# Kernel optimization log

Hardware: AMD Instinct MI355X
Metric: run time of the kernel (lower is better)

## Reference

```python
import jax, jax.numpy as jnp
import numpy as np

N = 100000
E = 1600000
G = 64  # number of graphs
H = 128
BN_EPS = 1e-5


def setup_inputs() -> dict:
    key = jax.random.key(0)
    ks = jax.random.split(key, 12)
    x = jax.random.normal(ks[0], (N, 3), dtype=jnp.float32)
    edge_index = jax.random.randint(ks[1], (2, E), 0, N, dtype=jnp.int64)
    batch = jnp.sort(jax.random.randint(ks[2], (N,), 0, G, dtype=jnp.int64))
    W1 = jax.random.normal(ks[3], (3, H), dtype=jnp.float32) * 0.3
    W2 = jax.random.normal(ks[4], (H, H), dtype=jnp.float32) * 0.05
    W3 = jax.random.normal(ks[5], (H, H), dtype=jnp.float32) * 0.05
    lin_W = jax.random.normal(ks[6], (H, 2), dtype=jnp.float32) * 0.05
    d = {
        'x': x, 'edge_index': edge_index, 'batch': batch,
        'W1': W1, 'b1': jnp.zeros((H,), jnp.float32),
        'W2': W2, 'b2': jnp.zeros((H,), jnp.float32),
        'W3': W3, 'b3': jnp.zeros((H,), jnp.float32),
        'lin_W': lin_W, 'lin_b': jnp.zeros((2,), jnp.float32),
    }
    for i, kk in zip((1, 2, 3), ks[7:10]):
        d[f'bn{i}_g'] = jnp.ones((H,), jnp.float32)
        d[f'bn{i}_b'] = jnp.zeros((H,), jnp.float32)
        d[f'bn{i}_m'] = jnp.zeros((H,), jnp.float32)
        d[f'bn{i}_v'] = jax.random.uniform(kk, (H,), dtype=jnp.float32, minval=0.5, maxval=1.5)
    return d


def _gcn(x, src, dst, norm, W, b):
    # GCNConv: out = scatter_add(norm * (xW)[src], dst) + b
    h = x @ W
    msg = h[src] * norm[:, None]
    agg = jax.ops.segment_sum(msg, dst, num_segments=N)
    return agg + b


def _bn_eval(x, g, b, m, v):
    return (x - m) * jax.lax.rsqrt(v + BN_EPS) * g + b


def reference(x, edge_index, batch, W1, b1, W2, b2, W3, b3,
              bn1_g, bn1_b, bn1_m, bn1_v,
              bn2_g, bn2_b, bn2_m, bn2_v,
              bn3_g, bn3_b, bn3_m, bn3_v,
              lin_W, lin_b):
    loop = jnp.arange(N, dtype=edge_index.dtype)
    src = jnp.concatenate([edge_index[0], loop])
    dst = jnp.concatenate([edge_index[1], loop])
    # symmetric normalization with self-loops: deg from destination nodes
    deg = jax.ops.segment_sum(jnp.ones_like(dst, dtype=x.dtype), dst, num_segments=N)
    dinv = jnp.where(deg > 0, jax.lax.rsqrt(deg), 0.0)
    norm = dinv[src] * dinv[dst]

    h = jax.nn.relu(_bn_eval(_gcn(x, src, dst, norm, W1, b1), bn1_g, bn1_b, bn1_m, bn1_v))
    h = jax.nn.relu(_bn_eval(_gcn(h, src, dst, norm, W2, b2), bn2_g, bn2_b, bn2_m, bn2_v))
    h = jax.nn.relu(_bn_eval(_gcn(h, src, dst, norm, W3, b3), bn3_g, bn3_b, bn3_m, bn3_v))
    # dropout is identity in eval mode
    sums = jax.ops.segment_sum(h, batch, num_segments=G)
    cnts = jax.ops.segment_sum(jnp.ones((N,), h.dtype), batch, num_segments=G)
    pooled = sums / jnp.maximum(cnts, 1.0)[:, None]
    return pooled @ lin_W + lin_b
```

## Files before the change

### kernel.cpp

```cpp
#include <hip/hip_runtime.h>

#define NN 100000
#define EE 1600000
#define GG 64
#define HH 128
#define BN_EPS 1e-5f

#define CB 782
#define NB 256
#define TILE 6250

typedef unsigned short ushort_t;

static __device__ inline ushort_t f2bf(float f) {
    unsigned u = __float_as_uint(f);
    unsigned r = (u + 0x7FFF + ((u >> 16) & 1)) >> 16;
    return (ushort_t)r;
}
static __device__ inline float bf2f(ushort_t b) {
    return __uint_as_float(((unsigned)b) << 16);
}


__global__ __launch_bounds__(256) void k_hist(const int* __restrict__ ei,
                                              int* __restrict__ histG) {
    __shared__ int h[CB];
    int t = threadIdx.x;
    for (int i = t; i < CB; i += 256) h[i] = 0;
    __syncthreads();
    int e0 = blockIdx.x * TILE;
    for (int i = t; i < TILE; i += 256) {
        int d = ei[EE + e0 + i];
        atomicAdd(&h[d >> 7], 1);
    }
    __syncthreads();
    for (int i = t; i < CB; i += 256) histG[blockIdx.x * CB + i] = h[i];
}

__global__ __launch_bounds__(NB) void k_bscan(int* __restrict__ histG,
                                              int* __restrict__ total) {
    __shared__ int sh[NB];
    int t = threadIdx.x;
    int c = blockIdx.x;
    sh[t] = histG[t * CB + c];
    __syncthreads();
    for (int d = 1; d < NB; d <<= 1) {
        int x = (t >= d) ? sh[t - d] : 0;
        __syncthreads();
        sh[t] += x;
        __syncthreads();
    }
    histG[t * CB + c] = (t > 0) ? sh[t - 1] : 0;
    if (t == NB - 1) total[c] = sh[NB - 1];
}

__global__ __launch_bounds__(1024) void k_cbase(const int* __restrict__ total,
                                                int* __restrict__ cbase) {
    __shared__ int sh[1024];
    int t = threadIdx.x;
    sh[t] = (t < CB) ? total[t] : 0;
    __syncthreads();
    for (int d = 1; d < 1024; d <<= 1) {
        int x = (t >= d) ? sh[t - d] : 0;
        __syncthreads();
        sh[t] += x;
        __syncthreads();
    }
    if (t < CB) cbase[t] = (t > 0) ? sh[t - 1] : 0;
    if (t == CB - 1) cbase[CB] = sh[t];
}

__global__ __launch_bounds__(256) void k_cscatter(const int* __restrict__ ei,
                                                  const int* __restrict__ histG,
                                                  const int* __restrict__ cbase,
                                                  int* __restrict__ metaS) {
    __shared__ int base_l[CB];
    __shared__ int cur_l[CB];
    int t = threadIdx.x;
    int b = blockIdx.x;
    for (int i = t; i < CB; i += 256) {
        base_l[i] = cbase[i] + histG[b * CB + i];
        cur_l[i] = 0;
    }
    __syncthreads();
    int e0 = b * TILE;
    for (int i = t; i < TILE; i += 256) {
        int s = ei[e0 + i];
        int d = ei[EE + e0 + i];
        int c = d >> 7;
        int p = base_l[c] + atomicAdd(&cur_l[c], 1);
        metaS[p] = s | ((d & 127) << 17);
    }
}

__global__ __launch_bounds__(256) void k_fine(const int* __restrict__ metaS,
                                              const int* __restrict__ cbase,
                                              int* __restrict__ cnt,
                                              int* __restrict__ offs,
                                              int* __restrict__ col,
                                              float* __restrict__ dinv) {
    __shared__ int hist[128];
    __shared__ int scn[128];
    __shared__ int cur[128];
    int t = threadIdx.x;
    int c = blockIdx.x;
    int lo = cbase[c], hi = cbase[c + 1];
    if (t < 128) hist[t] = 0;
    __syncthreads();
    for (int r = lo + t; r < hi; r += 256) atomicAdd(&hist[metaS[r] >> 17], 1);
    __syncthreads();
    if (t < 128) scn[t] = hist[t];
    __syncthreads();
    for (int d = 1; d < 128; d <<= 1) {
        int x = (t >= d && t < 128) ? scn[t - d] : 0;
        __syncthreads();
        if (t < 128) scn[t] += x;
        __syncthreads();
    }
    if (t < 128) {
        int excl = (t > 0) ? scn[t - 1] : 0;
        cur[t] = excl;
        int node = c * 128 + t;
        if (node < NN) {
            cnt[node] = hist[t];
            offs[node] = lo + excl;
            dinv[node] = rsqrtf((float)(hist[t] + 1));
        }
    }
    __syncthreads();
    for (int r = lo + t; r < hi; r += 256) {
        int pk = metaS[r];
        int s = pk & 0x1FFFF;
        int idx = atomicAdd(&cur[pk >> 17], 1);
        col[lo + idx] = s;
    }
}


__global__ __launch_bounds__(256) void k_aggx(const float* __restrict__ x,
                                              const int* __restrict__ offs,
                                              const int* __restrict__ cnt,
                                              const int* __restrict__ col,
                                              const float* __restrict__ dinv,
                                              float* __restrict__ wgt,
                                              float4* __restrict__ agg) {
    int tid = threadIdx.x;
    int wave = tid >> 6;
    int lane = tid & 63;
    int grp = lane >> 4;
    int l = lane & 15;
    int n = blockIdx.x * 16 + wave * 4 + grp;
    float dv = dinv[n];
    int base = offs[n], cn = cnt[n];
    float a0 = 0.f, a1 = 0.f, a2 = 0.f;
    for (int i = l; i < cn; i += 16) {
        int s = col[base + i];
        float w = dinv[s] * dv;
        wgt[base + i] = w;
        a0 += w * x[s * 3 + 0];
        a1 += w * x[s * 3 + 1];
        a2 += w * x[s * 3 + 2];
    }
#pragma unroll
    for (int off = 8; off >= 1; off >>= 1) {
        a0 += __shfl_xor(a0, off, 16);
        a1 += __shfl_xor(a1, off, 16);
        a2 += __shfl_xor(a2, off, 16);
    }
    if (l == 0) {
        float w0 = dv * dv;
        a0 += w0 * x[n * 3 + 0];
        a1 += w0 * x[n * 3 + 1];
        a2 += w0 * x[n * 3 + 2];
        agg[n] = make_float4(a0, a1, a2, 0.f);
    }
}


__global__ __launch_bounds__(256) void k_mml1(const float4* __restrict__ agg,
                                              const float* __restrict__ W1,
                                              const float* __restrict__ b1,
                                              const float* __restrict__ g1,
                                              const float* __restrict__ bb1,
                                              const float* __restrict__ m1,
                                              const float* __restrict__ v1,
                                              const float* __restrict__ W2,
                                              ushort_t* __restrict__ outB) {
    __shared__ float xs[64][132];
    __shared__ float4 ag[64];
    int tid = threadIdx.x;
    int row0 = blockIdx.x * 64;
    if (tid < 64) {
        int gr = row0 + tid;
        ag[tid] = (gr < NN) ? agg[gr] : make_float4(0.f, 0.f, 0.f, 0.f);
    }
    __syncthreads();
    {
        int c = tid & 127;
        int rh = tid >> 7;
        float w0 = W1[c], w1 = W1[128 + c], w2 = W1[256 + c];
        float sc = g1[c] * rsqrtf(v1[c] + BN_EPS);
        float sh = (b1[c] - m1[c]) * sc + bb1[c];
#pragma unroll
        for (int i = 0; i < 32; i++) {
            int r = 2 * i + rh;
            float4 a = ag[r];
            float t = a.x * w0 + a.y * w1 + a.z * w2;
            xs[r][c] = fmaxf(t * sc + sh, 0.f);
        }
    }
    __syncthreads();

    int tx = tid & 31;
    int ty = tid >> 5;
    float acc[8][4];
#pragma unroll
    for (int i = 0; i < 8; i++)
#pragma unroll
        for (int j = 0; j < 4; j++) acc[i][j] = 0.f;

    const float* Wp = W2 + tx * 4;
#pragma unroll 4
    for (int k = 0; k < 128; k++) {
        float4 w = *(const float4*)&Wp[k * HH];
#pragma unroll
        for (int i = 0; i < 8; i++) {
            float xv = xs[ty * 8 + i][k];
            acc[i][0] += xv * w.x;
            acc[i][1] += xv * w.y;
            acc[i][2] += xv * w.z;
            acc[i][3] += xv * w.w;
        }
    }
#pragma unroll
    for (int i = 0; i < 8; i++) {
        int gr = row0 + ty * 8 + i;
        if (gr < NN) {
            ushort4 o;
            o.x = f2bf(acc[i][0]);
            o.y = f2bf(acc[i][1]);
            o.z = f2bf(acc[i][2]);
            o.w = f2bf(acc[i][3]);
            *(ushort4*)&outB[(size_t)gr * HH + tx * 4] = o;
        }
    }
}


__global__ __launch_bounds__(256) void k_mm(const ushort_t* __restrict__ xin,
                                            const float* __restrict__ W,
                                            ushort_t* __restrict__ outB) {
    __shared__ float xs[64][132];
    int tid = threadIdx.x;
    int tx = tid & 31;
    int ty = tid >> 5;
    int row0 = blockIdx.x * 64;
#pragma unroll
    for (int i = 0; i < 4; i++) {
        int idx8 = i * 256 + tid;
        int r = idx8 >> 4;
        int k8 = (idx8 & 15) * 8;
        int gr = row0 + r;
        int4 pk = (gr < NN) ? *(const int4*)&xin[(size_t)gr * HH + k8]
                            : make_int4(0, 0, 0, 0);
        float* dst = &xs[r][k8];
        dst[0] = __uint_as_float(((unsigned)pk.x) << 16);
        dst[1] = __uint_as_float(((unsigned)pk.x) & 0xFFFF0000u);
        dst[2] = __uint_as_float(((unsigned)pk.y) << 16);
        dst[3] = __uint_as_float(((unsigned)pk.y) & 0xFFFF0000u);
        dst[4] = __uint_as_float(((unsigned)pk.z) << 16);
        dst[5] = __uint_as_float(((unsigned)pk.z) & 0xFFFF0000u);
        dst[6] = __uint_as_float(((unsigned)pk.w) << 16);
        dst[7] = __uint_as_float(((unsigned)pk.w) & 0xFFFF0000u);
    }
    __syncthreads();
    float acc[8][4];
#pragma unroll
    for (int i = 0; i < 8; i++)
#pragma unroll
        for (int j = 0; j < 4; j++) acc[i][j] = 0.f;

    const float* Wp = W + tx * 4;
#pragma unroll 4
    for (int k = 0; k < 128; k++) {
        float4 w = *(const float4*)&Wp[k * HH];
#pragma unroll
        for (int i = 0; i < 8; i++) {
            float xv = xs[ty * 8 + i][k];
            acc[i][0] += xv * w.x;
            acc[i][1] += xv * w.y;
            acc[i][2] += xv * w.z;
            acc[i][3] += xv * w.w;
        }
    }
#pragma unroll
    for (int i = 0; i < 8; i++) {
        int gr = row0 + ty * 8 + i;
        if (gr < NN) {
            ushort4 o;
            o.x = f2bf(acc[i][0]);
            o.y = f2bf(acc[i][1]);
            o.z = f2bf(acc[i][2]);
            o.w = f2bf(acc[i][3]);
            *(ushort4*)&outB[(size_t)gr * HH + tx * 4] = o;
        }
    }
}


__global__ __launch_bounds__(256) void k_agg(const ushort_t* __restrict__ t,
                                             const int* __restrict__ offs,
                                             const int* __restrict__ cnt,
                                             const int* __restrict__ col,
                                             const float* __restrict__ wgt,
                                             const float* __restrict__ dinv,
                                             const float* __restrict__ bias,
                                             const float* __restrict__ g,
                                             const float* __restrict__ bb,
                                             const float* __restrict__ m,
                                             const float* __restrict__ v,
                                             ushort_t* __restrict__ out) {
    int wave = threadIdx.x >> 6;
    int lane = threadIdx.x & 63;
    int half = lane >> 5;
    int l = lane & 31;
    int d = blockIdx.x * 8 + wave * 2 + half;
    int c0 = l * 4;
    float dv = dinv[d];
    float w0 = dv * dv;
    ushort4 selfR = *(const ushort4*)&t[(size_t)d * HH + c0];
    float4 acc;
    acc.x = bf2f(selfR.x) * w0; acc.y = bf2f(selfR.y) * w0;
    acc.z = bf2f(selfR.z) * w0; acc.w = bf2f(selfR.w) * w0;
    int base = offs[d], cn = cnt[d];
    for (int ib = 0; ib < cn; ib += 32) {
        int i = ib + l;
        int s = 0;
        float w = 0.f;
        if (i < cn) {
            s = col[base + i];
            w = wgt[base + i];
        }
        int lim = min(32, cn - ib);
#pragma unroll 8
        for (int j = 0; j < lim; j++) {
            int ss = __shfl(s, j, 32);
            float ww = __shfl(w, j, 32);
            ushort4 tv = *(const ushort4*)&t[(size_t)ss * HH + c0];
            acc.x += ww * bf2f(tv.x);
            acc.y += ww * bf2f(tv.y);
            acc.z += ww * bf2f(tv.z);
            acc.w += ww * bf2f(tv.w);
        }
    }
    float4 gg = *(const float4*)&g[c0];
    float4 vv = *(const float4*)&v[c0];
    float4 mm = *(const float4*)&m[c0];
    float4 bv = *(const float4*)&bb[c0];
    float4 bi = *(const float4*)&bias[c0];
    float sc0 = gg.x * rsqrtf(vv.x + BN_EPS);
    float sc1 = gg.y * rsqrtf(vv.y + BN_EPS);
    float sc2 = gg.z * rsqrtf(vv.z + BN_EPS);
    float sc3 = gg.w * rsqrtf(vv.w + BN_EPS);
    ushort4 o;
    o.x = f2bf(fmaxf(acc.x * sc0 + (bi.x - mm.x) * sc0 + bv.x, 0.f));
    o.y = f2bf(fmaxf(acc.y * sc1 + (bi.y - mm.y) * sc1 + bv.y, 0.f));
    o.z = f2bf(fmaxf(acc.z * sc2 + (bi.z - mm.z) * sc2 + bv.z, 0.f));
    o.w = f2bf(fmaxf(acc.w * sc3 + (bi.w - mm.w) * sc3 + bv.w, 0.f));
    *(ushort4*)&out[(size_t)d * HH + c0] = o;
}


#define PBLK 2048
__global__ void k_pool(const ushort_t* __restrict__ h, const int* __restrict__ batch,
                       float* __restrict__ gsum, int* __restrict__ gcnt) {
    int c = threadIdx.x;
    int per = (NN + PBLK - 1) / PBLK;
    int n0 = blockIdx.x * per;
    int n1 = min(NN, n0 + per);
    if (n0 >= NN) return;
    float acc = 0.f;
    int cur = batch[n0];
    int count = 0;
    for (int n = n0; n < n1; n++) {
        int gr = batch[n];
        if (gr != cur) {
            atomicAdd(&gsum[cur * HH + c], acc);
            if (c == 0) atomicAdd(&gcnt[cur], count);
            acc = 0.f; count = 0; cur = gr;
        }
        acc += bf2f(h[(size_t)n * HH + c]);
        count++;
    }
    atomicAdd(&gsum[cur * HH + c], acc);
    if (c == 0) atomicAdd(&gcnt[cur], count);
}

__global__ void k_head(const float* __restrict__ gsum, const int* __restrict__ gcnt,
                       const float* __restrict__ linW, const float* __restrict__ linb,
                       float* __restrict__ out) {
    int t = threadIdx.x;
    int gr = t >> 1, j = t & 1;
    float inv = 1.0f / fmaxf((float)gcnt[gr], 1.0f);
    float acc = 0.f;
    for (int c = 0; c < HH; c++) acc += gsum[gr * HH + c] * linW[c * 2 + j];
    out[t] = acc * inv + linb[j];
}


static inline size_t al256(size_t x) { return (x + 255) & ~(size_t)255; }

extern "C" void kernel_launch(void* const* d_in, const int* in_sizes, int n_in,
                              void* d_out, int out_size, void* d_ws, size_t ws_size,
                              hipStream_t stream) {
    const float* x    = (const float*)d_in[0];
    const int*   ei   = (const int*)d_in[1];
    const int*   batch= (const int*)d_in[2];
    const float* W1   = (const float*)d_in[3];
    const float* b1   = (const float*)d_in[4];
    const float* W2   = (const float*)d_in[5];
    const float* b2   = (const float*)d_in[6];
    const float* W3   = (const float*)d_in[7];
    const float* b3   = (const float*)d_in[8];
    const float* linW = (const float*)d_in[9];
    const float* linb = (const float*)d_in[10];
    const float* bn1g = (const float*)d_in[11];
    const float* bn1b = (const float*)d_in[12];
    const float* bn1m = (const float*)d_in[13];
    const float* bn1v = (const float*)d_in[14];
    const float* bn2g = (const float*)d_in[15];
    const float* bn2b = (const float*)d_in[16];
    const float* bn2m = (const float*)d_in[17];
    const float* bn2v = (const float*)d_in[18];
    const float* bn3g = (const float*)d_in[19];
    const float* bn3b = (const float*)d_in[20];
    const float* bn3m = (const float*)d_in[21];
    const float* bn3v = (const float*)d_in[22];
    float* out = (float*)d_out;

    char* ws = (char*)d_ws;
    size_t off = 0;
    int*    histG  = (int*)(ws + off);    off += al256((size_t)NB * CB * 4);
    int*    total  = (int*)(ws + off);    off += al256((size_t)CB * 4);
    int*    cbase  = (int*)(ws + off);    off += al256((size_t)(CB + 1) * 4);
    int*    cnt    = (int*)(ws + off);    off += al256((size_t)NN * 4);
    int*    offs   = (int*)(ws + off);    off += al256((size_t)NN * 4);
    float*  dinv   = (float*)(ws + off);  off += al256((size_t)NN * 4);
    int*    col    = (int*)(ws + off);    off += al256((size_t)EE * 4);
    float*  wgt    = (float*)(ws + off);  off += al256((size_t)EE * 4);
    float4* agg    = (float4*)(ws + off); off += al256((size_t)NN * 16);
    char*   bufA   = (char*)(ws + off);   off += al256((size_t)NN * HH * 2);
    char*   bufB   = (char*)(ws + off);   off += al256((size_t)NN * HH * 4);
    float*  gsum   = (float*)(ws + off);  off += (size_t)GG * HH * 4;
    int*    gcnt   = (int*)(ws + off);    off += al256((size_t)GG * 4);

    int* metaS = (int*)bufB;
    ushort_t* tB = (ushort_t*)bufB;
    ushort_t* hB = (ushort_t*)bufA;

    hipMemsetAsync(gsum, 0, (size_t)GG * HH * 4 + (size_t)GG * 4, stream);

    k_hist<<<NB, 256, 0, stream>>>(ei, histG);
    k_bscan<<<CB, NB, 0, stream>>>(histG, total);
    k_cbase<<<1, 1024, 0, stream>>>(total, cbase);
    k_cscatter<<<NB, 256, 0, stream>>>(ei, histG, cbase, metaS);
    k_fine<<<CB, 256, 0, stream>>>(metaS, cbase, cnt, offs, col, dinv);

    k_aggx<<<NN / 16, 256, 0, stream>>>(x, offs, cnt, col, dinv, wgt, agg);

    k_mml1<<<(NN + 63) / 64, 256, 0, stream>>>(agg, W1, b1, bn1g, bn1b, bn1m, bn1v,
                                               W2, tB);
    k_agg<<<NN / 8, 256, 0, stream>>>(tB, offs, cnt, col, wgt, dinv,
                                      b2, bn2g, bn2b, bn2m, bn2v, hB);

    k_mm<<<(NN + 63) / 64, 256, 0, stream>>>(hB, W3, tB);
    k_agg<<<NN / 8, 256, 0, stream>>>(tB, offs, cnt, col, wgt, dinv,
                                      b3, bn3g, bn3b, bn3m, bn3v, hB);

    k_pool<<<PBLK, 128, 0, stream>>>(hB, batch, gsum, gcnt);
    k_head<<<1, 128, 0, stream>>>(gsum, gcnt, linW, linb, out);
}
```

Measured before the change: 441.4 us.

## Use bf16 MFMA for dense layers, fuse pooling into last aggregation

Replaces the FP32 scalar GEMMs in the layer-1 and layer-3 matmul kernels with bf16 MFMA 16x16x32, using a split hi/lo bf16 representation to keep near-FP32 accuracy. Weights are pre-split into fragment layout by a new prep kernel. The aggregation kernel is restructured so each wave walks a contiguous range of nodes, with 16 lanes covering 128 channels and 4 neighbor groups. It computes edge weights on the fly instead of storing and reloading a wgt array, and the final layer's mean pooling is fused into it, removing the pool kernel. The extra MFMA passes for precision splitting and per-element scalar output stores add cost in exchange.

```diff
diff --git a/kernel.cpp b/kernel.cpp
--- a/kernel.cpp
+++ b/kernel.cpp
@@ -11,6 +11,12 @@
 #define TILE 6250
 
 typedef unsigned short ushort_t;
+typedef __attribute__((ext_vector_type(8))) short bf16x8;
+typedef __attribute__((ext_vector_type(4))) float f32x4;
+
+#define MFMA16 __builtin_amdgcn_mfma_f32_16x16x32_bf16
+
+#define WFRAG_LO 16384
 
 static __device__ inline ushort_t f2bf(float f) {
     unsigned u = __float_as_uint(f);
@@ -20,6 +26,8 @@
 static __device__ inline float bf2f(ushort_t b) {
     return __uint_as_float(((unsigned)b) << 16);
 }
+#define BFLO(u) __uint_as_float(((unsigned)(u)) << 16)
+#define BFHI(u) __uint_as_float(((unsigned)(u)) & 0xFFFF0000u)
 
 
 __global__ __launch_bounds__(256) void k_hist(const int* __restrict__ ei,
@@ -137,12 +145,43 @@
 }
 
 
+__global__ __launch_bounds__(256) void k_gcnt(const int* __restrict__ batch,
+                                              int* __restrict__ gcnt) {
+    int i = blockIdx.x * 256 + threadIdx.x;
+    if (i < NN) atomicAdd(&gcnt[batch[i]], 1);
+}
+
+
+__global__ __launch_bounds__(256) void k_wprep(const float* __restrict__ W2,
+                                               const float* __restrict__ W3,
+                                               ushort_t* __restrict__ w2f,
+                                               ushort_t* __restrict__ w3f) {
+    const float* W = (blockIdx.x & 8) ? W3 : W2;
+    ushort_t* o = (blockIdx.x & 8) ? w3f : w2f;
+    int tid = ((int)blockIdx.x & 7) * 256 + threadIdx.x;
+    int l = tid & 63;
+    int kb = ((tid >> 6) & 3) * 32 + (l >> 4) * 8;
+    int n = (tid >> 8) * 16 + (l & 15);
+    unsigned hp[4], lp[4];
+#pragma unroll
+    for (int p = 0; p < 4; p++) {
+        float v0 = W[(size_t)(kb + 2 * p) * HH + n];
+        float v1 = W[(size_t)(kb + 2 * p + 1) * HH + n];
+        ushort_t h0 = f2bf(v0), h1 = f2bf(v1);
+        ushort_t l0 = f2bf(v0 - bf2f(h0)), l1 = f2bf(v1 - bf2f(h1));
+        hp[p] = (unsigned)h0 | ((unsigned)h1 << 16);
+        lp[p] = (unsigned)l0 | ((unsigned)l1 << 16);
+    }
+    *(uint4*)&o[(size_t)tid * 8] = make_uint4(hp[0], hp[1], hp[2], hp[3]);
+    *(uint4*)&o[WFRAG_LO + (size_t)tid * 8] = make_uint4(lp[0], lp[1], lp[2], lp[3]);
+}
+
+
 __global__ __launch_bounds__(256) void k_aggx(const float* __restrict__ x,
                                               const int* __restrict__ offs,
                                               const int* __restrict__ cnt,
                                               const int* __restrict__ col,
                                               const float* __restrict__ dinv,
-                                              float* __restrict__ wgt,
                                               float4* __restrict__ agg) {
     int tid = threadIdx.x;
     int wave = tid >> 6;
@@ -156,7 +195,6 @@
     for (int i = l; i < cn; i += 16) {
         int s = col[base + i];
         float w = dinv[s] * dv;
-        wgt[base + i] = w;
         a0 += w * x[s * 3 + 0];
         a1 += w * x[s * 3 + 1];
         a2 += w * x[s * 3 + 2];
@@ -184,10 +222,10 @@
                                               const float* __restrict__ bb1,
                                               const float* __restrict__ m1,
                                               const float* __restrict__ v1,
-                                              const float* __restrict__ W2,
+                                              const ushort_t* __restrict__ Wf,
                                               ushort_t* __restrict__ outB) {
-    __shared__ float xs[64][132];
     __shared__ float4 ag[64];
+    __shared__ __align__(16) ushort_t xh[2][64 * HH];
     int tid = threadIdx.x;
     int row0 = blockIdx.x * 64;
     if (tid < 64) {
@@ -205,196 +243,229 @@
         for (int i = 0; i < 32; i++) {
             int r = 2 * i + rh;
             float4 a = ag[r];
-            float t = a.x * w0 + a.y * w1 + a.z * w2;
-            xs[r][c] = fmaxf(t * sc + sh, 0.f);
-        }
-    }
-    __syncthreads();
-
-    int tx = tid & 31;
-    int ty = tid >> 5;
-    float acc[8][4];
-#pragma unroll
-    for (int i = 0; i < 8; i++)
-#pragma unroll
-        for (int j = 0; j < 4; j++) acc[i][j] = 0.f;
-
-    const float* Wp = W2 + tx * 4;
-#pragma unroll 4
-    for (int k = 0; k < 128; k++) {
-        float4 w = *(const float4*)&Wp[k * HH];
-#pragma unroll
-        for (int i = 0; i < 8; i++) {
-            float xv = xs[ty * 8 + i][k];
-            acc[i][0] += xv * w.x;
-            acc[i][1] += xv * w.y;
-            acc[i][2] += xv * w.z;
-            acc[i][3] += xv * w.w;
-        }
-    }
-#pragma unroll
-    for (int i = 0; i < 8; i++) {
-        int gr = row0 + ty * 8 + i;
+            float t = fmaxf((a.x * w0 + a.y * w1 + a.z * w2) * sc + sh, 0.f);
+            ushort_t hi = f2bf(t);
+            ushort_t lo = f2bf(t - bf2f(hi));
+            int idx = r * HH + (c ^ ((r & 7) << 3));
+            xh[0][idx] = hi;
+            xh[1][idx] = lo;
+        }
+    }
+    __syncthreads();
+
+    int w = tid >> 6, l = tid & 63;
+    int r_lo = l & 15, kgrp = l >> 4;
+    int row_l = w * 16 + r_lo;
+    f32x4 acc[8];
+#pragma unroll
+    for (int nt = 0; nt < 8; nt++) acc[nt] = (f32x4){0.f, 0.f, 0.f, 0.f};
+
+#pragma unroll
+    for (int kk = 0; kk < 4; kk++) {
+        int ke = kk * 32 + kgrp * 8;
+        int idx = row_l * HH + (ke ^ ((row_l & 7) << 3));
+        bf16x8 ahf = *(const bf16x8*)&xh[0][idx];
+        bf16x8 alf = *(const bf16x8*)&xh[1][idx];
+#pragma unroll
+        for (int nt = 0; nt < 8; nt++) {
+            int fo = ((((nt << 2) | kk) << 6) + l) * 8;
+            bf16x8 bh = *(const bf16x8*)&Wf[fo];
+            bf16x8 bl = *(const bf16x8*)&Wf[WFRAG_LO + fo];
+            acc[nt] = MFMA16(ahf, bh, acc[nt], 0, 0, 0);
+            acc[nt] = MFMA16(ahf, bl, acc[nt], 0, 0, 0);
+            acc[nt] = MFMA16(alf, bh, acc[nt], 0, 0, 0);
+        }
+    }
+#pragma unroll
+    for (int q = 0; q < 4; q++) {
+        int gr = row0 + w * 16 + kgrp * 4 + q;
         if (gr < NN) {
-            ushort4 o;
-            o.x = f2bf(acc[i][0]);
-            o.y = f2bf(acc[i][1]);
-            o.z = f2bf(acc[i][2]);
-            o.w = f2bf(acc[i][3]);
-            *(ushort4*)&outB[(size_t)gr * HH + tx * 4] = o;
+            size_t rb = (size_t)gr * HH + r_lo;
+#pragma unroll
+            for (int nt = 0; nt < 8; nt++)
+                outB[rb + nt * 16] = f2bf(acc[nt][q]);
         }
     }
 }
 
 
 __global__ __launch_bounds__(256) void k_mm(const ushort_t* __restrict__ xin,
-                                            const float* __restrict__ W,
+                                            const ushort_t* __restrict__ Wf,
                                             ushort_t* __restrict__ outB) {
-    __shared__ float xs[64][132];
     int tid = threadIdx.x;
-    int tx = tid & 31;
-    int ty = tid >> 5;
-    int row0 = blockIdx.x * 64;
-#pragma unroll
-    for (int i = 0; i < 4; i++) {
-        int idx8 = i * 256 + tid;
-        int r = idx8 >> 4;
-        int k8 = (idx8 & 15) * 8;
-        int gr = row0 + r;
-        int4 pk = (gr < NN) ? *(const int4*)&xin[(size_t)gr * HH + k8]
-                            : make_int4(0, 0, 0, 0);
-        float* dst = &xs[r][k8];
-        dst[0] = __uint_as_float(((unsigned)pk.x) << 16);
-        dst[1] = __uint_as_float(((unsigned)pk.x) & 0xFFFF0000u);
-        dst[2] = __uint_as_float(((unsigned)pk.y) << 16);
-        dst[3] = __uint_as_float(((unsigned)pk.y) & 0xFFFF0000u);
-        dst[4] = __uint_as_float(((unsigned)pk.z) << 16);
-        dst[5] = __uint_as_float(((unsigned)pk.z) & 0xFFFF0000u);
-        dst[6] = __uint_as_float(((unsigned)pk.w) << 16);
-        dst[7] = __uint_as_float(((unsigned)pk.w) & 0xFFFF0000u);
-    }
-    __syncthreads();
-    float acc[8][4];
-#pragma unroll
-    for (int i = 0; i < 8; i++)
-#pragma unroll
-        for (int j = 0; j < 4; j++) acc[i][j] = 0.f;
-
-    const float* Wp = W + tx * 4;
-#pragma unroll 4
-    for (int k = 0; k < 128; k++) {
-        float4 w = *(const float4*)&Wp[k * HH];
-#pragma unroll
-        for (int i = 0; i < 8; i++) {
-            float xv = xs[ty * 8 + i][k];
-            acc[i][0] += xv * w.x;
-            acc[i][1] += xv * w.y;
-            acc[i][2] += xv * w.z;
-            acc[i][3] += xv * w.w;
-        }
-    }
-#pragma unroll
-    for (int i = 0; i < 8; i++) {
-        int gr = row0 + ty * 8 + i;
-        if (gr < NN) {
-            ushort4 o;
-            o.x = f2bf(acc[i][0]);
-            o.y = f2bf(acc[i][1]);
-            o.z = f2bf(acc[i][2]);
-            o.w = f2bf(acc[i][3]);
-            *(ushort4*)&outB[(size_t)gr * HH + tx * 4] = o;
-        }
-    }
-}
-
-
+    int w = tid >> 6, l = tid & 63;
+    int row0 = blockIdx.x * 128 + w * 32;
+    int r_lo = l & 15, kgrp = l >> 4;
+    f32x4 acc[2][8];
+#pragma unroll
+    for (int rt = 0; rt < 2; rt++)
+#pragma unroll
+        for (int nt = 0; nt < 8; nt++) acc[rt][nt] = (f32x4){0.f, 0.f, 0.f, 0.f};
+
+    bf16x8 za = {0, 0, 0, 0, 0, 0, 0, 0};
+#pragma unroll
+    for (int kk = 0; kk < 4; kk++) {
+        int ke = kk * 32 + kgrp * 8;
+        int ra0 = row0 + r_lo;
+        int ra1 = row0 + 16 + r_lo;
+        bf16x8 a0 = (ra0 < NN) ? *(const bf16x8*)&xin[(size_t)ra0 * HH + ke] : za;
+        bf16x8 a1 = (ra1 < NN) ? *(const bf16x8*)&xin[(size_t)ra1 * HH + ke] : za;
+#pragma unroll
+        for (int nt = 0; nt < 8; nt++) {
+            int fo = ((((nt << 2) | kk) << 6) + l) * 8;
+            bf16x8 bh = *(const bf16x8*)&Wf[fo];
+            bf16x8 bl = *(const bf16x8*)&Wf[WFRAG_LO + fo];
+            acc[0][nt] = MFMA16(a0, bh, acc[0][nt], 0, 0, 0);
+            acc[0][nt] = MFMA16(a0, bl, acc[0][nt], 0, 0, 0);
+            acc[1][nt] = MFMA16(a1, bh, acc[1][nt], 0, 0, 0);
+            acc[1][nt] = MFMA16(a1, bl, acc[1][nt], 0, 0, 0);
+        }
+    }
+#pragma unroll
+    for (int rt = 0; rt < 2; rt++)
+#pragma unroll
+        for (int q = 0; q < 4; q++) {
+            int gr = row0 + rt * 16 + kgrp * 4 + q;
+            if (gr < NN) {
+                size_t rb = (size_t)gr * HH + r_lo;
+#pragma unroll
+                for (int nt = 0; nt < 8; nt++)
+                    outB[rb + nt * 16] = f2bf(acc[rt][nt][q]);
+            }
+        }
+}
+
+
+template<int POOL>
 __global__ __launch_bounds__(256) void k_agg(const ushort_t* __restrict__ t,
                                              const int* __restrict__ offs,
                                              const int* __restrict__ cnt,
                                              const int* __restrict__ col,
-                                             const float* __restrict__ wgt,
                                              const float* __restrict__ dinv,
+                                             const int* __restrict__ batch,
                                              const float* __restrict__ bias,
                                              const float* __restrict__ g,
                                              const float* __restrict__ bb,
                                              const float* __restrict__ m,
                                              const float* __restrict__ v,
-                                             ushort_t* __restrict__ out) {
-    int wave = threadIdx.x >> 6;
-    int lane = threadIdx.x & 63;
-    int half = lane >> 5;
-    int l = lane & 31;
-    int d = blockIdx.x * 8 + wave * 2 + half;
-    int c0 = l * 4;
-    float dv = dinv[d];
-    float w0 = dv * dv;
-    ushort4 selfR = *(const ushort4*)&t[(size_t)d * HH + c0];
-    float4 acc;
-    acc.x = bf2f(selfR.x) * w0; acc.y = bf2f(selfR.y) * w0;
-    acc.z = bf2f(selfR.z) * w0; acc.w = bf2f(selfR.w) * w0;
-    int base = offs[d], cn = cnt[d];
-    for (int ib = 0; ib < cn; ib += 32) {
-        int i = ib + l;
-        int s = 0;
-        float w = 0.f;
-        if (i < cn) {
-            s = col[base + i];
-            w = wgt[base + i];
-        }
-        int lim = min(32, cn - ib);
-#pragma unroll 8
-        for (int j = 0; j < lim; j++) {
-            int ss = __shfl(s, j, 32);
-            float ww = __shfl(w, j, 32);
-            ushort4 tv = *(const ushort4*)&t[(size_t)ss * HH + c0];
-            acc.x += ww * bf2f(tv.x);
-            acc.y += ww * bf2f(tv.y);
-            acc.z += ww * bf2f(tv.z);
-            acc.w += ww * bf2f(tv.w);
-        }
-    }
-    float4 gg = *(const float4*)&g[c0];
-    float4 vv = *(const float4*)&v[c0];
-    float4 mm = *(const float4*)&m[c0];
-    float4 bv = *(const float4*)&bb[c0];
-    float4 bi = *(const float4*)&bias[c0];
-    float sc0 = gg.x * rsqrtf(vv.x + BN_EPS);
-    float sc1 = gg.y * rsqrtf(vv.y + BN_EPS);
-    float sc2 = gg.z * rsqrtf(vv.z + BN_EPS);
-    float sc3 = gg.w * rsqrtf(vv.w + BN_EPS);
-    ushort4 o;
-    o.x = f2bf(fmaxf(acc.x * sc0 + (bi.x - mm.x) * sc0 + bv.x, 0.f));
-    o.y = f2bf(fmaxf(acc.y * sc1 + (bi.y - mm.y) * sc1 + bv.y, 0.f));
-    o.z = f2bf(fmaxf(acc.z * sc2 + (bi.z - mm.z) * sc2 + bv.z, 0.f));
-    o.w = f2bf(fmaxf(acc.w * sc3 + (bi.w - mm.w) * sc3 + bv.w, 0.f));
-    *(ushort4*)&out[(size_t)d * HH + c0] = o;
-}
-
-
-#define PBLK 2048
-__global__ void k_pool(const ushort_t* __restrict__ h, const int* __restrict__ batch,
-                       float* __restrict__ gsum, int* __restrict__ gcnt) {
-    int c = threadIdx.x;
-    int per = (NN + PBLK - 1) / PBLK;
-    int n0 = blockIdx.x * per;
-    int n1 = min(NN, n0 + per);
-    if (n0 >= NN) return;
-    float acc = 0.f;
-    int cur = batch[n0];
-    int count = 0;
-    for (int n = n0; n < n1; n++) {
-        int gr = batch[n];
-        if (gr != cur) {
-            atomicAdd(&gsum[cur * HH + c], acc);
-            if (c == 0) atomicAdd(&gcnt[cur], count);
-            acc = 0.f; count = 0; cur = gr;
-        }
-        acc += bf2f(h[(size_t)n * HH + c]);
-        count++;
-    }
-    atomicAdd(&gsum[cur * HH + c], acc);
-    if (c == 0) atomicAdd(&gcnt[cur], count);
-}
+                                             ushort_t* __restrict__ out,
+                                             float* __restrict__ gsum) {
+    int l = threadIdx.x & 63;
+    int nw = gridDim.x << 2;
+    int wid = ((int)blockIdx.x << 2) + (threadIdx.x >> 6);
+    int grp = l >> 4, sub = l & 15;
+    int c0 = sub << 3;
+    float sc[8], sh[8];
+#pragma unroll
+    for (int e = 0; e < 8; e++) {
+        int c = c0 + e;
+        float s_ = g[c] * rsqrtf(v[c] + BN_EPS);
+        sc[e] = s_;
+        sh[e] = (bias[c] - m[c]) * s_ + bb[c];
+    }
+    int chunk = (NN + nw - 1) / nw;
+    int d0 = wid * chunk;
+    int d1 = min(NN, d0 + chunk);
+    float pacc[8];
+    int curg = -1;
+    if (POOL) {
+#pragma unroll
+        for (int e = 0; e < 8; e++) pacc[e] = 0.f;
+        if (d0 < d1) curg = batch[d0];
+    }
+    for (int d = d0; d < d1; d++) {
+        float dv = dinv[d];
+        int base = offs[d], cn = cnt[d];
+        float acc[8];
+        if (grp == 0) {
+            float w0 = dv * dv;
+            const int4 pk = *(const int4*)&t[(size_t)d * HH + c0];
+            acc[0] = w0 * BFLO(pk.x); acc[1] = w0 * BFHI(pk.x);
+            acc[2] = w0 * BFLO(pk.y); acc[3] = w0 * BFHI(pk.y);
+            acc[4] = w0 * BFLO(pk.z); acc[5] = w0 * BFHI(pk.z);
+            acc[6] = w0 * BFLO(pk.w); acc[7] = w0 * BFHI(pk.w);
+        } else {
+#pragma unroll
+            for (int e = 0; e < 8; e++) acc[e] = 0.f;
+        }
+        for (int cb = 0; cb < cn; cb += 64) {
+            int ce = min(64, cn - cb);
+            int sv = 0;
+            float wv = 0.f;
+            if (l < ce) {
+                sv = col[base + cb + l];
+                wv = dinv[sv] * dv;
+            }
+            int cf = ce & ~3;
+#pragma unroll 4
+            for (int e0 = 0; e0 < cf; e0 += 4) {
+                int ss = __shfl(sv, e0 + grp, 64);
+                float ww = __shfl(wv, e0 + grp, 64);
+                const int4 pk = *(const int4*)&t[(size_t)ss * HH + c0];
+                acc[0] += ww * BFLO(pk.x); acc[1] += ww * BFHI(pk.x);
+                acc[2] += ww * BFLO(pk.y); acc[3] += ww * BFHI(pk.y);
+                acc[4] += ww * BFLO(pk.z); acc[5] += ww * BFHI(pk.z);
+                acc[6] += ww * BFLO(pk.w); acc[7] += ww * BFHI(pk.w);
+            }
+            if (cf < ce) {
+                int idx = cf + grp;
+                int ss = __shfl(sv, idx, 64);
+                float ww = __shfl(wv, idx, 64);
+                if (idx < ce) {
+                    const int4 pk = *(const int4*)&t[(size_t)ss * HH + c0];
+                    acc[0] += ww * BFLO(pk.x); acc[1] += ww * BFHI(pk.x);
+                    acc[2] += ww * BFLO(pk.y); acc[3] += ww * BFHI(pk.y);
+                    acc[4] += ww * BFLO(pk.z); acc[5] += ww * BFHI(pk.z);
+                    acc[6] += ww * BFLO(pk.w); acc[7] += ww * BFHI(pk.w);
+                }
+            }
+        }
+#pragma unroll
+        for (int e = 0; e < 8; e++) {
+            acc[e] += __shfl_xor(acc[e], 16, 64);
+            acc[e] += __shfl_xor(acc[e], 32, 64);
+        }
+        if (POOL) {
+            int gnow = batch[d];
+            if (gnow != curg) {
+                if (l < 16) {
+#pragma unroll
+                    for (int e = 0; e < 8; e++)
+                        atomicAdd(&gsum[curg * HH + c0 + e], pacc[e]);
+                }
+#pragma unroll
+                for (int e = 0; e < 8; e++) pacc[e] = 0.f;
+                curg = gnow;
+            }
+#pragma unroll
+            for (int e = 0; e < 8; e++)
+                pacc[e] += fmaxf(acc[e] * sc[e] + sh[e], 0.f);
+        } else {
+            if (l < 16) {
+                float r0 = fmaxf(acc[0] * sc[0] + sh[0], 0.f);
+                float r1 = fmaxf(acc[1] * sc[1] + sh[1], 0.f);
+                float r2 = fmaxf(acc[2] * sc[2] + sh[2], 0.f);
+                float r3 = fmaxf(acc[3] * sc[3] + sh[3], 0.f);
+                float r4 = fmaxf(acc[4] * sc[4] + sh[4], 0.f);
+                float r5 = fmaxf(acc[5] * sc[5] + sh[5], 0.f);
+                float r6 = fmaxf(acc[6] * sc[6] + sh[6], 0.f);
+                float r7 = fmaxf(acc[7] * sc[7] + sh[7], 0.f);
+                int4 o;
+                o.x = (int)f2bf(r0) | ((int)f2bf(r1) << 16);
+                o.y = (int)f2bf(r2) | ((int)f2bf(r3) << 16);
+                o.z = (int)f2bf(r4) | ((int)f2bf(r5) << 16);
+                o.w = (int)f2bf(r6) | ((int)f2bf(r7) << 16);
+                *(int4*)&out[(size_t)d * HH + c0] = o;
+            }
+        }
+    }
+    if (POOL && curg >= 0 && l < 16) {
+#pragma unroll
+        for (int e = 0; e < 8; e++)
+            atomicAdd(&gsum[curg * HH + c0 + e], pacc[e]);
+    }
+}
+
 
 __global__ void k_head(const float* __restrict__ gsum, const int* __restrict__ gcnt,
                        const float* __restrict__ linW, const float* __restrict__ linb,
@@ -447,7 +518,8 @@
     int*    offs   = (int*)(ws + off);    off += al256((size_t)NN * 4);
     float*  dinv   = (float*)(ws + off);  off += al256((size_t)NN * 4);
     int*    col    = (int*)(ws + off);    off += al256((size_t)EE * 4);
-    float*  wgt    = (float*)(ws + off);  off += al256((size_t)EE * 4);
+    ushort_t* w2f  = (ushort_t*)(ws + off); off += al256((size_t)2 * WFRAG_LO * 2);
+    ushort_t* w3f  = (ushort_t*)(ws + off); off += al256((size_t)2 * WFRAG_LO * 2);
     float4* agg    = (float4*)(ws + off); off += al256((size_t)NN * 16);
     char*   bufA   = (char*)(ws + off);   off += al256((size_t)NN * HH * 2);
     char*   bufB   = (char*)(ws + off);   off += al256((size_t)NN * HH * 4);
@@ -460,23 +532,25 @@
 
     hipMemsetAsync(gsum, 0, (size_t)GG * HH * 4 + (size_t)GG * 4, stream);
 
+    k_wprep<<<16, 256, 0, stream>>>(W2, W3, w2f, w3f);
+    k_gcnt<<<(NN + 255) / 256, 256, 0, stream>>>(batch, gcnt);
+
     k_hist<<<NB, 256, 0, stream>>>(ei, histG);
     k_bscan<<<CB, NB, 0, stream>>>(histG, total);
     k_cbase<<<1, 1024, 0, stream>>>(total, cbase);
     k_cscatter<<<NB, 256, 0, stream>>>(ei, histG, cbase, metaS);
     k_fine<<<CB, 256, 0, stream>>>(metaS, cbase, cnt, offs, col, dinv);
 
-    k_aggx<<<NN / 16, 256, 0, stream>>>(x, offs, cnt, col, dinv, wgt, agg);
+    k_aggx<<<NN / 16, 256, 0, stream>>>(x, offs, cnt, col, dinv, agg);
 
     k_mml1<<<(NN + 63) / 64, 256, 0, stream>>>(agg, W1, b1, bn1g, bn1b, bn1m, bn1v,
-                                               W2, tB);
-    k_agg<<<NN / 8, 256, 0, stream>>>(tB, offs, cnt, col, wgt, dinv,
-                                      b2, bn2g, bn2b, bn2m, bn2v, hB);
-
-    k_mm<<<(NN + 63) / 64, 256, 0, stream>>>(hB, W3, tB);
-    k_agg<<<NN / 8, 256, 0, stream>>>(tB, offs, cnt, col, wgt, dinv,
-                                      b3, bn3g, bn3b, bn3m, bn3v, hB);
-
-    k_pool<<<PBLK, 128, 0, stream>>>(hB, batch, gsum, gcnt);
+                                               w2f, tB);
+    k_agg<0><<<2048, 256, 0, stream>>>(tB, offs, cnt, col, dinv, batch,
+                                       b2, bn2g, bn2b, bn2m, bn2v, hB, nullptr);
+
+    k_mm<<<(NN + 127) / 128, 256, 0, stream>>>(hB, w3f, tB);
+    k_agg<1><<<2048, 256, 0, stream>>>(tB, offs, cnt, col, dinv, batch,
+                                       b3, bn3g, bn3b, bn3m, bn3v, nullptr, gsum);
+
     k_head<<<1, 128, 0, stream>>>(gsum, gcnt, linW, linb, out);
 }
```

Result: slower. 968.1 us (+119.3%).
